# Optimization experiments

Measured on AMD Instinct MI355X. Metric: run time of the kernel, lower is better.

The kernel has to match this reference:

```python
import jax, jax.numpy as jnp
from jax import lax
import numpy as np

B, N, C, HEADS = 8, 4096, 512, 16
HD = C // HEADS


def rope2d(x, h, w, base=10000.0):
    # x: [b, h, w, c]; 2D axial RoPE as in the torch `rope` helper
    c = x.shape[-1]
    k_max = c // 4  # feature_dim // (2 * len(channel_dims))
    theta = 1.0 / (base ** (jnp.arange(k_max, dtype=jnp.float32) / k_max))  # [k_max]
    ii = jnp.arange(h, dtype=jnp.float32)[:, None, None]  # row index
    jj = jnp.arange(w, dtype=jnp.float32)[None, :, None]  # col index
    ang = jnp.concatenate([
        jnp.broadcast_to(ii * theta, (h, w, k_max)),
        jnp.broadcast_to(jj * theta, (h, w, k_max)),
    ], axis=-1)  # [h, w, c//2]
    cos, sin = jnp.cos(ang), jnp.sin(ang)
    xp = x.reshape(x.shape[0], h, w, c // 2, 2)
    xr, xi = xp[..., 0], xp[..., 1]
    out = jnp.stack([xr * cos - xi * sin, xi * cos + xr * sin], axis=-1)
    return out.reshape(x.shape)


def setup_inputs() -> dict:
    key = jax.random.key(0)
    k1, k2, k3, k4, k5 = jax.random.split(key, 5)
    x = jax.random.normal(k1, (B, N, C), dtype=jnp.float32)
    Wqk = jax.random.normal(k2, (C, 2 * C), dtype=jnp.float32) * 0.02
    bqk = jax.random.normal(k3, (2 * C,), dtype=jnp.float32) * 0.02
    lepe_w = jax.random.normal(k4, (C, 1, 3, 3), dtype=jnp.float32) * 0.05  # depthwise OIHW
    lepe_b = jax.random.normal(k5, (C,), dtype=jnp.float32) * 0.02
    return {"x": x, "h": 64, "w": 64, "Wqk": Wqk, "bqk": bqk, "lepe_w": lepe_w, "lepe_b": lepe_b}


def reference(x, h, w, Wqk, bqk, lepe_w, lepe_b):
    b, n, c = x.shape
    hd = c // HEADS
    qk = x @ Wqk + bqk                       # [b, n, 2c]
    q = jax.nn.elu(qk[..., :c]) + 1.0        # ELU+1 feature map
    k = jax.nn.elu(qk[..., c:]) + 1.0
    v = x
    q_rope = rope2d(q.reshape(b, h, w, c), h, w).reshape(b, n, HEADS, hd)
    k_rope = rope2d(k.reshape(b, h, w, c), h, w).reshape(b, n, HEADS, hd)
    qh = q.reshape(b, n, HEADS, hd)
    kh = k.reshape(b, n, HEADS, hd)
    vh = v.reshape(b, n, HEADS, hd)
    k_mean = kh.mean(axis=1)                 # [b, HEADS, hd]
    z = 1.0 / (jnp.einsum('bnhd,bhd->bnh', qh, k_mean) + 1e-6)  # [b, n, HEADS]
    inv_n = 1.0 / jnp.float32(n)
    kv = jnp.einsum('bnhd,bnhe->bhde', k_rope, vh) * inv_n       # [b, HEADS, hd, hd]
    attn = jnp.einsum('bnhd,bhde->bnhe', q_rope, kv) * z[..., None]
    out = attn.reshape(b, n, c)
    # depthwise 3x3 LePE on v (== x) as NCHW image
    v_img = x.reshape(b, h, w, c).transpose(0, 3, 1, 2)
    lepe = lax.conv_general_dilated(v_img, lepe_w, (1, 1), 'SAME',
                                    feature_group_count=c,
                                    dimension_numbers=('NCHW', 'OIHW', 'NCHW'))
    lepe = lepe + lepe_b[None, :, None, None]
    out = out + lepe.transpose(0, 2, 3, 1).reshape(b, n, c)
    return out
```

## Files before the change

### kernel.cpp

```cpp
#include <hip/hip_runtime.h>
#include <stdint.h>

static constexpr int BATCH = 8;
static constexpr int NTOK  = 4096;
static constexpr int CDIM  = 512;
static constexpr int NCOL  = 1024;
static constexpr int MROWS = BATCH * NTOK;
static constexpr int KDIM  = 512;

static constexpr size_t OFF_KSUM = 0;
static constexpr size_t OFF_KV   = 16384;
static constexpr size_t OFF_XB   = 540672;
static constexpr size_t OFF_WT   = OFF_XB + 33554432;
static constexpr size_t OFF_QP   = OFF_WT + 1048576;
static constexpr size_t OFF_KR   = OFF_QP + 33554432;
static constexpr size_t OFF_TRIG = OFF_KR + 33554432;
static constexpr size_t OFF_WT9  = OFF_TRIG + 65536;
static constexpr size_t WS_NEED  = OFF_WT9 + 18432;

static constexpr int KV_CHUNKS = 64;
static constexpr int KV_OUT    = BATCH * 16 * 32 * 32;

typedef __attribute__((ext_vector_type(8))) short bf16x8;
typedef __attribute__((ext_vector_type(4))) float f32x4;
typedef __attribute__((ext_vector_type(8))) unsigned short u16x8;

__device__ __forceinline__ float bf2f(unsigned short u) {
  union { unsigned int i; float f; } v; v.i = ((unsigned int)u) << 16; return v.f;
}
__device__ __forceinline__ unsigned short f2bf(float f) {
  union { float f; unsigned int i; } v; v.f = f;
  unsigned int b = v.i + 0x7FFFu + ((v.i >> 16) & 1u);
  return (unsigned short)(b >> 16);
}
__device__ __forceinline__ void gload16(const void* g, void* l) {
  __builtin_amdgcn_global_load_lds(
      (const __attribute__((address_space(1))) unsigned int*)g,
      (__attribute__((address_space(3))) unsigned int*)l,
      16, 0, 0);
}
__device__ __forceinline__ float elu1(float v) {
  return v > 0.f ? v + 1.f : __expf(v);
}

__global__ void prep_kernel(const float* __restrict__ x, const float* __restrict__ Wqk,
                            const float* __restrict__ lepe_w,
                            float* __restrict__ wsf, unsigned short* __restrict__ xb,
                            unsigned short* __restrict__ wT, float2* __restrict__ trig,
                            float* __restrict__ wt9) {
  const int ZN = (int)(OFF_XB / 4);
  const int XN = MROWS * CDIM / 8;
  const int WN = (KDIM * NCOL) / 8;
  const int TN = 64 * 128;
  const int W9 = 9 * 512;
  const int total = ZN + XN + WN + TN + W9;
  for (int i = blockIdx.x * blockDim.x + threadIdx.x; i < total;
       i += gridDim.x * blockDim.x) {
    if (i < ZN) {
      wsf[i] = 0.f;
    } else if (i < ZN + XN) {
      const int j = i - ZN;
      const float4* xp = (const float4*)x + (size_t)j * 2;
      const float4 a = xp[0], b4 = xp[1];
      u16x8 o;
      o[0] = f2bf(a.x);  o[1] = f2bf(a.y);  o[2] = f2bf(a.z);  o[3] = f2bf(a.w);
      o[4] = f2bf(b4.x); o[5] = f2bf(b4.y); o[6] = f2bf(b4.z); o[7] = f2bf(b4.w);
      *((u16x8*)xb + j) = o;
    } else if (i < ZN + XN + WN) {
      const int j = i - ZN - XN;
      const int nc8 = j & 127;
      const int k   = j >> 7;
      const float4* wp = (const float4*)(Wqk + (size_t)k * NCOL + nc8 * 8);
      const float4 a = wp[0], b4 = wp[1];
      const float vals[8] = {a.x, a.y, a.z, a.w, b4.x, b4.y, b4.z, b4.w};
      const int nc0 = nc8 * 8;
#pragma unroll
      for (int t = 0; t < 8; ++t) wT[(size_t)(nc0 + t) * KDIM + k] = f2bf(vals[t]);
    } else if (i < ZN + XN + WN + TN) {
      const int j = i - ZN - XN - WN;
      const int tt = j & 127;
      const int pos = j >> 7;
      const float theta = __expf(-(float)tt * 0.07195578415f);
      const float ang = (float)pos * theta;
      float s, c;
      sincosf(ang, &s, &c);
      trig[pos * 128 + tt] = make_float2(c, s);
    } else {
      const int j = i - ZN - XN - WN - TN;
      const int tap = j >> 9;
      const int c   = j & 511;
      wt9[tap * 512 + c] = lepe_w[c * 9 + tap];
    }
  }
}

__global__ __launch_bounds__(256)
void gemm_kernel(const unsigned short* __restrict__ xb, const unsigned short* __restrict__ wT,
                 const float* __restrict__ bqk, const float2* __restrict__ trig,
                 unsigned short* __restrict__ qp, unsigned short* __restrict__ kr,
                 float* __restrict__ ksum) {
  __shared__ __align__(16) unsigned short Ab[128 * 32];
  __shared__ __align__(16) unsigned short Bt[128 * 32];
  __shared__ __align__(16) float Cst[32 * 132];
  const int tid = threadIdx.x;
  const int w = tid >> 6;
  const int l = tid & 63;
  const int m0 = blockIdx.x * 128;
  const int n0 = blockIdx.y * 128;
  const int wr = w >> 1, wc = w & 1;

  f32x4 acc[4][4];
#pragma unroll
  for (int i = 0; i < 4; ++i)
#pragma unroll
    for (int j = 0; j < 4; ++j) acc[i][j] = (f32x4){0.f, 0.f, 0.f, 0.f};

  const int c0 = w * 2, c1 = w * 2 + 1;
  const int lr = l >> 2;
  const int lk = (l & 3) * 8;
  const int la = l & 15, lg = l >> 4;
  const int lb = lg * 8;

  for (int kt = 0; kt < KDIM / 32; ++kt) {
    const int kc = kt * 32 + lk;
    gload16(xb + (size_t)(m0 + c0 * 16 + lr) * KDIM + kc, Ab + c0 * 512);
    gload16(xb + (size_t)(m0 + c1 * 16 + lr) * KDIM + kc, Ab + c1 * 512);
    gload16(wT + (size_t)(n0 + c0 * 16 + lr) * KDIM + kc, Bt + c0 * 512);
    gload16(wT + (size_t)(n0 + c1 * 16 + lr) * KDIM + kc, Bt + c1 * 512);
    __syncthreads();
    bf16x8 af[4], bfr[4];
#pragma unroll
    for (int mi = 0; mi < 4; ++mi)
      af[mi] = *(const bf16x8*)&Ab[(wr * 64 + mi * 16 + la) * 32 + lb];
#pragma unroll
    for (int ni = 0; ni < 4; ++ni)
      bfr[ni] = *(const bf16x8*)&Bt[(wc * 64 + ni * 16 + la) * 32 + lb];
#pragma unroll
    for (int mi = 0; mi < 4; ++mi)
#pragma unroll
      for (int ni = 0; ni < 4; ++ni)
        acc[mi][ni] = __builtin_amdgcn_mfma_f32_16x16x32_bf16(af[mi], bfr[ni], acc[mi][ni], 0, 0, 0);
    __syncthreads();
  }

  const bool isq = (blockIdx.y < 4);
  const int bidx = m0 >> 12;
  float colsum[4] = {0.f, 0.f, 0.f, 0.f};
#pragma unroll
  for (int ni = 0; ni < 4; ++ni) {
    const int colg = n0 + wc * 64 + ni * 16 + la;
    const float bias = bqk[colg];
#pragma unroll
    for (int mi = 0; mi < 4; ++mi) {
#pragma unroll
      for (int r = 0; r < 4; ++r) {
        const float v = elu1(acc[mi][ni][r] + bias);
        acc[mi][ni][r] = v;
        if (!isq) colsum[ni] += v;
      }
    }
  }
  if (!isq) {
#pragma unroll
    for (int ni = 0; ni < 4; ++ni) {
      float s = colsum[ni];
      s += __shfl_xor(s, 16);
      s += __shfl_xor(s, 32);
      if (lg == 0) {
        const int ck = n0 - 512 + wc * 64 + ni * 16 + la;
        atomicAdd(&ksum[bidx * CDIM + ck], s);
      }
    }
  }

  for (int cc = 0; cc < 4; ++cc) {
    __syncthreads();
    if (wr == (cc >> 1)) {
      const int mi0 = (cc & 1) * 2;
#pragma unroll
      for (int mil = 0; mil < 2; ++mil) {
#pragma unroll
        for (int ni = 0; ni < 4; ++ni) {
#pragma unroll
          for (int r = 0; r < 4; ++r) {
            Cst[(mil * 16 + lg * 4 + r) * 132 + wc * 64 + ni * 16 + la] = acc[mi0 + mil][ni][r];
          }
        }
      }
    }
    __syncthreads();
#pragma unroll
    for (int it = 0; it < 2; ++it) {
      const int idx = it * 256 + tid;
      const int rowloc = idx >> 4;
      const int seg = idx & 15;
      const int grow = m0 + cc * 32 + rowloc;
      const int lcol = seg * 8;
      float v[8];
      *(float2*)&v[0] = *(const float2*)&Cst[rowloc * 132 + lcol + 0];
      *(float2*)&v[2] = *(const float2*)&Cst[rowloc * 132 + lcol + 2];
      *(float2*)&v[4] = *(const float2*)&Cst[rowloc * 132 + lcol + 4];
      *(float2*)&v[6] = *(const float2*)&Cst[rowloc * 132 + lcol + 6];
      if (isq) {
        u16x8 o;
#pragma unroll
        for (int j = 0; j < 8; ++j) o[j] = f2bf(v[j]);
        *(u16x8*)(qp + (size_t)grow * CDIM + n0 + lcol) = o;
      } else {
        const int ck0 = n0 - 512 + lcol;
        const int n = grow & (NTOK - 1);
        const int p0 = ck0 >> 1;
        const int pos = (p0 >= 128) ? (n & 63) : (n >> 6);
        const float4 t01 = *(const float4*)&trig[pos * 128 + p0];
        const float4 t23 = *(const float4*)&trig[pos * 128 + p0 + 2];
        u16x8 o;
        o[0] = f2bf(v[0] * t01.x - v[1] * t01.y);
        o[1] = f2bf(v[1] * t01.x + v[0] * t01.y);
        o[2] = f2bf(v[2] * t01.z - v[3] * t01.w);
        o[3] = f2bf(v[3] * t01.z + v[2] * t01.w);
        o[4] = f2bf(v[4] * t23.x - v[5] * t23.y);
        o[5] = f2bf(v[5] * t23.x + v[4] * t23.y);
        o[6] = f2bf(v[6] * t23.z - v[7] * t23.w);
        o[7] = f2bf(v[7] * t23.z + v[6] * t23.w);
        *(u16x8*)(kr + (size_t)grow * CDIM + ck0) = o;
      }
    }
  }
}

__global__ __launch_bounds__(256)
void kvpart_kernel(const unsigned short* __restrict__ kr, const unsigned short* __restrict__ xb,
                   float* __restrict__ part) {
  const int bid = blockIdx.x;
  const int b = bid >> 6, ch = bid & 63;
  const int t = threadIdx.x;
  const int h = t >> 4;
  const int sub = t & 15;
  const int d0 = (sub >> 2) * 8, e0 = (sub & 3) * 8;

  float acc[8][8];
#pragma unroll
  for (int i = 0; i < 8; ++i)
#pragma unroll
    for (int j = 0; j < 8; ++j) acc[i][j] = 0.f;

  const size_t rowbase = (size_t)(b * NTOK + ch * 64) * CDIM + h * 32;
#pragma unroll 2
  for (int r = 0; r < 64; ++r) {
    const size_t off = rowbase + (size_t)r * CDIM;
    const u16x8 k8 = *(const u16x8*)(kr + off + d0);
    const u16x8 v8 = *(const u16x8*)(xb + off + e0);
    float kf[8], vf[8];
#pragma unroll
    for (int i = 0; i < 8; ++i) { kf[i] = bf2f(k8[i]); vf[i] = bf2f(v8[i]); }
#pragma unroll
    for (int i = 0; i < 8; ++i)
#pragma unroll
      for (int j = 0; j < 8; ++j) acc[i][j] += kf[i] * vf[j];
  }

  float* p = part + ((size_t)ch * BATCH * 16 + b * 16 + h) * 1024;
#pragma unroll
  for (int i = 0; i < 8; ++i) {
    *(float4*)&p[(d0 + i) * 32 + e0 + 0] = *(float4*)&acc[i][0];
    *(float4*)&p[(d0 + i) * 32 + e0 + 4] = *(float4*)&acc[i][4];
  }
}

__global__ __launch_bounds__(256)
void kvred_kernel(const float* __restrict__ part, float* __restrict__ kv) {
  const int o = blockIdx.x * 256 + threadIdx.x;
  float s0 = 0.f, s1 = 0.f, s2 = 0.f, s3 = 0.f;
#pragma unroll
  for (int ch = 0; ch < KV_CHUNKS; ch += 4) {
    s0 += part[(size_t)(ch + 0) * KV_OUT + o];
    s1 += part[(size_t)(ch + 1) * KV_OUT + o];
    s2 += part[(size_t)(ch + 2) * KV_OUT + o];
    s3 += part[(size_t)(ch + 3) * KV_OUT + o];
  }
  kv[o] = (s0 + s1 + s2 + s3) * (1.0f / (float)NTOK);
}

__global__ __launch_bounds__(256)
void out4_kernel(const unsigned short* __restrict__ qp, const float* __restrict__ ksum,
                 const float* __restrict__ kv, const float2* __restrict__ trig,
                 const unsigned short* __restrict__ xb, const float* __restrict__ wt9,
                 const float* __restrict__ lepe_b, float* __restrict__ out) {
  __shared__ __align__(16) float kvs[32 * 32];
  __shared__ __align__(16) float qrs[32 * 40];
  const int y = blockIdx.x;
  const int h = blockIdx.y >> 1, half = blockIdx.y & 1;
  const int b = blockIdx.z;
  const int t = threadIdx.x;
  const int e8 = t & 7, tok = t >> 3;
  const int c4 = e8 * 4;

  ((float4*)kvs)[t] = ((const float4*)(kv + (size_t)(b * 16 + h) * 1024))[t];

  const float4 ks4 = *(const float4*)(ksum + b * CDIM + h * 32 + c4);
  const float4 lb4 = *(const float4*)(lepe_b + h * 32 + c4);
  float4 w4[9];
#pragma unroll
  for (int tap = 0; tap < 9; ++tap)
    w4[tap] = *(const float4*)(wt9 + tap * CDIM + h * 32 + c4);
  const int pbase = (h * 16 + e8 * 2) & 127;
  __syncthreads();

  const float inv_n = 1.0f / (float)NTOK;
  const int col = half * 32 + tok;
  const int n = y * 64 + col;
  const size_t rowoff = ((size_t)(b * NTOK + n)) * CDIM + h * 32;

  const ushort4 q4u = *(const ushort4*)(qp + rowoff + c4);
  const float q0 = bf2f(q4u.x), q1 = bf2f(q4u.y), q2 = bf2f(q4u.z), q3 = bf2f(q4u.w);
  float zs = q0 * ks4.x + q1 * ks4.y + q2 * ks4.z + q3 * ks4.w;
  zs += __shfl_xor(zs, 1);
  zs += __shfl_xor(zs, 2);
  zs += __shfl_xor(zs, 4);
  const float z = 1.0f / (zs * inv_n + 1e-6f);
  const int pos = (h >= 8) ? col : y;
  const float4 cs01 = *(const float4*)&trig[pos * 128 + pbase];
  float4 qr;
  qr.x = q0 * cs01.x - q1 * cs01.y;
  qr.y = q1 * cs01.x + q0 * cs01.y;
  qr.z = q2 * cs01.z - q3 * cs01.w;
  qr.w = q3 * cs01.z + q2 * cs01.w;
  *(float4*)&qrs[tok * 40 + c4] = qr;
  float4 acc = lb4;
#pragma unroll
  for (int dy = 0; dy < 3; ++dy) {
    const int iy = y + dy - 1;
    if (iy < 0 || iy > 63) continue;
#pragma unroll
    for (int dx = 0; dx < 3; ++dx) {
      const int ix = col + dx - 1;
      if (ix < 0 || ix > 63) continue;
      const ushort4 xv = *(const ushort4*)(xb + ((size_t)(b * NTOK) + iy * 64 + ix) * CDIM + h * 32 + c4);
      const float4 wv = w4[dy * 3 + dx];
      acc.x += bf2f(xv.x) * wv.x; acc.y += bf2f(xv.y) * wv.y;
      acc.z += bf2f(xv.z) * wv.z; acc.w += bf2f(xv.w) * wv.w;
    }
  }
  float4 attn = {0.f, 0.f, 0.f, 0.f};
#pragma unroll
  for (int dg = 0; dg < 8; ++dg) {
    const float4 qv = *(const float4*)&qrs[tok * 40 + dg * 4];
#pragma unroll
    for (int j = 0; j < 4; ++j) {
      const float qs = (j == 0) ? qv.x : (j == 1) ? qv.y : (j == 2) ? qv.z : qv.w;
      const float4 kvr = *(const float4*)&kvs[(dg * 4 + j) * 32 + c4];
      attn.x += qs * kvr.x; attn.y += qs * kvr.y;
      attn.z += qs * kvr.z; attn.w += qs * kvr.w;
    }
  }
  float4 res;
  res.x = attn.x * z + acc.x;
  res.y = attn.y * z + acc.y;
  res.z = attn.z * z + acc.z;
  res.w = attn.w * z + acc.w;
  *(float4*)(out + rowoff + c4) = res;
}

extern "C" void kernel_launch(void* const* d_in, const int* in_sizes, int n_in,
                              void* d_out, int out_size, void* d_ws, size_t ws_size,
                              hipStream_t stream) {
  const float* x      = (const float*)d_in[0];
  const float* Wqk    = (const float*)d_in[3];
  const float* bqk    = (const float*)d_in[4];
  const float* lepe_w = (const float*)d_in[5];
  const float* lepe_b = (const float*)d_in[6];
  float* out = (float*)d_out;

  if (ws_size < WS_NEED) return;

  char* ws = (char*)d_ws;
  float* ksum            = (float*)(ws + OFF_KSUM);
  float* kv              = (float*)(ws + OFF_KV);
  unsigned short* xb     = (unsigned short*)(ws + OFF_XB);
  unsigned short* wT     = (unsigned short*)(ws + OFF_WT);
  unsigned short* qp     = (unsigned short*)(ws + OFF_QP);
  unsigned short* kr     = (unsigned short*)(ws + OFF_KR);
  float2* trig           = (float2*)(ws + OFF_TRIG);
  float* wt9             = (float*)(ws + OFF_WT9);
  float* part            = (float*)d_out;

  hipLaunchKernelGGL(prep_kernel, dim3(2048), dim3(256), 0, stream,
                     x, Wqk, lepe_w, (float*)ws, xb, wT, trig, wt9);
  hipLaunchKernelGGL(gemm_kernel, dim3(MROWS / 128, NCOL / 128), dim3(256), 0, stream,
                     xb, wT, bqk, trig, qp, kr, ksum);
  hipLaunchKernelGGL(kvpart_kernel, dim3(BATCH * KV_CHUNKS), dim3(256), 0, stream,
                     kr, xb, part);
  hipLaunchKernelGGL(kvred_kernel, dim3(KV_OUT / 256), dim3(256), 0, stream,
                     part, kv);
  hipLaunchKernelGGL(out4_kernel, dim3(64, 32, 8), dim3(256), 0, stream,
                     qp, ksum, kv, trig, xb, wt9, lepe_b, out);
}
```

Measured before the change: 183.0 us.

## Double-buffer GEMM LDS tiles and remap block order for A-tile reuse

Moves the GEMM's shared-memory staging to two buffers, so the next K-slice is prefetched while MFMAs run on the current one. The epilogue's Cst scratch now aliases the staging buffers, which keeps total LDS use from growing much. Block indices are also linearized so the 8 N-tiles of one M-tile are scheduled next to each other, which should improve L2 reuse of the x rows. One barrier per iteration is removed, but correctness now depends on the trailing sync before Cst reuses the buffers.

```diff
diff --git a/kernel.cpp b/kernel.cpp
--- a/kernel.cpp
+++ b/kernel.cpp
@@ -99,14 +99,15 @@
                  const float* __restrict__ bqk, const float2* __restrict__ trig,
                  unsigned short* __restrict__ qp, unsigned short* __restrict__ kr,
                  float* __restrict__ ksum) {
-  __shared__ __align__(16) unsigned short Ab[128 * 32];
-  __shared__ __align__(16) unsigned short Bt[128 * 32];
-  __shared__ __align__(16) float Cst[32 * 132];
+  __shared__ __align__(16) unsigned short S[2][2][128 * 32];
+  float* Cst = (float*)&S[0][0][0];
   const int tid = threadIdx.x;
   const int w = tid >> 6;
   const int l = tid & 63;
-  const int m0 = blockIdx.x * 128;
-  const int n0 = blockIdx.y * 128;
+  const int d = blockIdx.x + blockIdx.y * 256;
+  const int m0 = (d >> 3) * 128;
+  const int nidx = d & 7;
+  const int n0 = nidx * 128;
   const int wr = w >> 1, wc = w & 1;
 
   f32x4 acc[4][4];
@@ -121,20 +122,26 @@
   const int la = l & 15, lg = l >> 4;
   const int lb = lg * 8;
 
+#define STAGE(kt, bb) do {                                                        \
+    const int kc_ = (kt) * 32 + lk;                                               \
+    gload16(xb + (size_t)(m0 + c0 * 16 + lr) * KDIM + kc_, &S[bb][0][c0 * 512]);  \
+    gload16(xb + (size_t)(m0 + c1 * 16 + lr) * KDIM + kc_, &S[bb][0][c1 * 512]);  \
+    gload16(wT + (size_t)(n0 + c0 * 16 + lr) * KDIM + kc_, &S[bb][1][c0 * 512]);  \
+    gload16(wT + (size_t)(n0 + c1 * 16 + lr) * KDIM + kc_, &S[bb][1][c1 * 512]);  \
+  } while (0)
+
+  STAGE(0, 0);
+  __syncthreads();
   for (int kt = 0; kt < KDIM / 32; ++kt) {
-    const int kc = kt * 32 + lk;
-    gload16(xb + (size_t)(m0 + c0 * 16 + lr) * KDIM + kc, Ab + c0 * 512);
-    gload16(xb + (size_t)(m0 + c1 * 16 + lr) * KDIM + kc, Ab + c1 * 512);
-    gload16(wT + (size_t)(n0 + c0 * 16 + lr) * KDIM + kc, Bt + c0 * 512);
-    gload16(wT + (size_t)(n0 + c1 * 16 + lr) * KDIM + kc, Bt + c1 * 512);
-    __syncthreads();
+    const int cur = kt & 1;
+    if (kt < KDIM / 32 - 1) STAGE(kt + 1, cur ^ 1);
     bf16x8 af[4], bfr[4];
 #pragma unroll
     for (int mi = 0; mi < 4; ++mi)
-      af[mi] = *(const bf16x8*)&Ab[(wr * 64 + mi * 16 + la) * 32 + lb];
+      af[mi] = *(const bf16x8*)&S[cur][0][(wr * 64 + mi * 16 + la) * 32 + lb];
 #pragma unroll
     for (int ni = 0; ni < 4; ++ni)
-      bfr[ni] = *(const bf16x8*)&Bt[(wc * 64 + ni * 16 + la) * 32 + lb];
+      bfr[ni] = *(const bf16x8*)&S[cur][1][(wc * 64 + ni * 16 + la) * 32 + lb];
 #pragma unroll
     for (int mi = 0; mi < 4; ++mi)
 #pragma unroll
@@ -142,8 +149,9 @@
         acc[mi][ni] = __builtin_amdgcn_mfma_f32_16x16x32_bf16(af[mi], bfr[ni], acc[mi][ni], 0, 0, 0);
     __syncthreads();
   }
-
-  const bool isq = (blockIdx.y < 4);
+#undef STAGE
+
+  const bool isq = (nidx < 4);
   const int bidx = m0 >> 12;
   float colsum[4] = {0.f, 0.f, 0.f, 0.f};
 #pragma unroll
```

After: 189.5 us. +3.5%, slower.
